# Kernel tuning notes

Measured on AMD Instinct MI355X. Metric: run time of the kernel, lower is better.

The kernel has to match this reference:

```python
import jax, jax.numpy as jnp
import numpy as np

N, D_IN, F1, F2, D_OUT = 10000, 128, 20, 20, 128

def setup_inputs() -> dict:
    key = jax.random.key(0)
    ks = jax.random.split(key, 8)
    x = jax.random.normal(ks[0], (N, D_IN), dtype=jnp.float32)
    adj = jax.random.uniform(ks[1], (N, N), dtype=jnp.float32)
    # Kipf-style GraphConvolution params: W in [in,out], bias [out]
    def glorot(k, fi, fo):
        s = 1.0 / np.sqrt(fi)
        return jax.random.uniform(k, (fi, fo), dtype=jnp.float32, minval=-s, maxval=s)
    W1 = glorot(ks[2], D_IN, F1); b1 = jnp.zeros((F1,), jnp.float32)
    W2 = glorot(ks[3], F1, F2);  b2 = jnp.zeros((F2,), jnp.float32)
    W3 = glorot(ks[4], F2, D_OUT); b3 = jnp.zeros((D_OUT,), jnp.float32)
    return {"x": x, "adj": adj, "W1": W1, "b1": b1, "W2": W2, "b2": b2, "W3": W3, "b3": b3}

def _gcn(h, adj, W, b):
    # GraphConvolution: adj @ (h @ W) + b
    return adj @ (h @ W) + b

def reference(x, adj, W1, b1, W2, b2, W3, b3):
    # eval mode: F.dropout(training=False) is identity
    h = jax.nn.relu(_gcn(x, adj, W1, b1))
    h = jax.nn.relu(_gcn(h, adj, W2, b2))
    h = jax.nn.relu(_gcn(h, adj, W3, b3))
    return jax.nn.relu(h + x)
```

## Files before the change

kernel.cpp:

```cpp
#include <hip/hip_runtime.h>

constexpr int NN   = 10000;
constexpr int DIN  = 128;
constexpr int F    = 20;
constexpr int DOUT = 128;

constexpr int KSPLIT = 25;
constexpr int KRANGE = NN / KSPLIT;
constexpr int TM     = 128;
constexpr int ROWBLK = (NN + TM - 1) / TM;
constexpr int NFLT4  = NN * F / 4;

__global__ __launch_bounds__(256) void gemm_x_w1(const float* __restrict__ x,
                                                 const float* __restrict__ W,
                                                 float* __restrict__ out) {
    int t = blockIdx.x * 256 + threadIdx.x;
    if (t >= NN * F) return;
    int i = t / F, f = t % F;
    const float4* xp = (const float4*)(x + (size_t)i * DIN);
    float s = 0.f;
#pragma unroll
    for (int k4 = 0; k4 < DIN / 4; ++k4) {
        float4 xv = xp[k4];
        int k = k4 * 4;
        s += xv.x * W[(k + 0) * F + f];
        s += xv.y * W[(k + 1) * F + f];
        s += xv.z * W[(k + 2) * F + f];
        s += xv.w * W[(k + 3) * F + f];
    }
    out[t] = s;
}

__global__ __launch_bounds__(256) void gemm_h_w2(const float* __restrict__ h,
                                                 const float* __restrict__ W,
                                                 float* __restrict__ out) {
    int t = blockIdx.x * 256 + threadIdx.x;
    if (t >= NN * F) return;
    int i = t / F, g = t % F;
    const float* hp = h + (size_t)i * F;
    float s = 0.f;
#pragma unroll
    for (int f = 0; f < F; ++f) s += hp[f] * W[f * F + g];
    out[t] = s;
}

__global__ __launch_bounds__(256) void bias_relu(const float* __restrict__ in,
                                                 const float* __restrict__ b,
                                                 float* __restrict__ out) {
    int t = blockIdx.x * 256 + threadIdx.x;
    if (t >= NN * F) return;
    out[t] = fmaxf(in[t] + b[t % F], 0.f);
}

template <int REV, int PART>
__global__ __launch_bounds__(256) void adjmm(const float* __restrict__ adj,
                                             const float* __restrict__ t,
                                             float* __restrict__ out) {
    __shared__ __align__(16) float tl[KRANGE * F];

    const int tid = threadIdx.x;
    const int bx = REV ? ((int)gridDim.x - 1 - (int)blockIdx.x) : (int)blockIdx.x;
    const int by = REV ? ((int)gridDim.y - 1 - (int)blockIdx.y) : (int)blockIdx.y;
    const int row0 = bx * TM;
    const int k0   = by * KRANGE;

    {
        const float4* src = (const float4*)(t + (size_t)k0 * F);
        float4* dst = (float4*)tl;
#pragma unroll
        for (int i = 0; i < 8; ++i) {
            int idx = tid + i * 256;
            if (idx < KRANGE * F / 4) dst[idx] = src[idx];
        }
    }
    __syncthreads();

    const int r   = tid >> 1;
    const int p   = tid & 1;
    const int row = row0 + r;
    if (row < NN) {
        float4 acc[5];
#pragma unroll
        for (int c = 0; c < 5; ++c) acc[c] = make_float4(0.f, 0.f, 0.f, 0.f);

        const float4* ap = (const float4*)(adj + (size_t)row * NN + k0);
#pragma unroll 2
        for (int m = 0; m < KRANGE / 8; ++m) {
            const int mm = REV ? (KRANGE / 8 - 1 - m) : m;
            float4 a = ap[2 * mm + p];
            const float* trow = tl + (8 * mm + 4 * p) * F;
#pragma unroll
            for (int j = 0; j < 4; ++j) {
                const float aj = (j == 0) ? a.x : (j == 1) ? a.y : (j == 2) ? a.z : a.w;
                const float4* tp = (const float4*)(trow + j * F);
#pragma unroll
                for (int c = 0; c < 5; ++c) {
                    float4 tv = tp[c];
                    acc[c].x += aj * tv.x;
                    acc[c].y += aj * tv.y;
                    acc[c].z += aj * tv.z;
                    acc[c].w += aj * tv.w;
                }
            }
        }

#pragma unroll
        for (int c = 0; c < 5; ++c) {
            acc[c].x += __shfl_xor(acc[c].x, 1);
            acc[c].y += __shfl_xor(acc[c].y, 1);
            acc[c].z += __shfl_xor(acc[c].z, 1);
            acc[c].w += __shfl_xor(acc[c].w, 1);
        }

        if (PART) {
            if (p == 0) {
                float4* op = (float4*)(out + ((size_t)by * NN + row) * F);
#pragma unroll
                for (int c = 0; c < 5; ++c) op[c] = acc[c];
            }
        } else {
            if (p == 0) {
                float* op = out + (size_t)row * F;
#pragma unroll
                for (int c = 0; c < 5; ++c) {
                    atomicAdd(op + c * 4 + 0, acc[c].x);
                    atomicAdd(op + c * 4 + 1, acc[c].y);
                    atomicAdd(op + c * 4 + 2, acc[c].z);
                    atomicAdd(op + c * 4 + 3, acc[c].w);
                }
            }
        }
    }
}

template <int BIASRELU>
__global__ __launch_bounds__(256) void reduce_p(const float* __restrict__ P,
                                                const float* __restrict__ b,
                                                float* __restrict__ out) {
    int t = blockIdx.x * 256 + threadIdx.x;
    if (t >= NFLT4) return;
    float4 s = ((const float4*)P)[t];
    for (int k = 1; k < KSPLIT; ++k) {
        float4 v = ((const float4*)P)[(size_t)k * NFLT4 + t];
        s.x += v.x; s.y += v.y; s.z += v.z; s.w += v.w;
    }
    if (BIASRELU) {
        int f4 = t % (F / 4);
        float4 bv = ((const float4*)b)[f4];
        s.x = fmaxf(s.x + bv.x, 0.f);
        s.y = fmaxf(s.y + bv.y, 0.f);
        s.z = fmaxf(s.z + bv.z, 0.f);
        s.w = fmaxf(s.w + bv.w, 0.f);
    }
    ((float4*)out)[t] = s;
}

__global__ __launch_bounds__(256) void final_fuse(const float* __restrict__ u,
                                                  const float* __restrict__ W3,
                                                  const float* __restrict__ b3,
                                                  const float* __restrict__ x,
                                                  float* __restrict__ out) {
    int t = blockIdx.x * 256 + threadIdx.x;
    if (t >= NN * DOUT) return;
    int i = t / DOUT, f = t % DOUT;
    const float* up = u + (size_t)i * F;
    float s = b3[f];
#pragma unroll
    for (int g = 0; g < F; ++g) s += up[g] * W3[g * DOUT + f];
    float h = fmaxf(s, 0.f);
    out[t] = fmaxf(h + x[t], 0.f);
}

extern "C" void kernel_launch(void* const* d_in, const int* in_sizes, int n_in,
                              void* d_out, int out_size, void* d_ws, size_t ws_size,
                              hipStream_t stream) {
    const float* x   = (const float*)d_in[0];
    const float* adj = (const float*)d_in[1];
    const float* W1  = (const float*)d_in[2];
    const float* b1  = (const float*)d_in[3];
    const float* W2  = (const float*)d_in[4];
    const float* b2  = (const float*)d_in[5];
    const float* W3  = (const float*)d_in[6];
    const float* b3  = (const float*)d_in[7];
    float* out = (float*)d_out;

    float* A = (float*)d_ws;
    float* C = A + (size_t)NN * F;
    float* P = C + (size_t)NN * F;
    const size_t nf_bytes = (size_t)NN * F * sizeof(float);
    const size_t need = nf_bytes * (2 + KSPLIT);

    const int blk_nf  = (NN * F + 255) / 256;
    const int blk_nf4 = (NFLT4 + 255) / 256;
    const int blk_no  = (NN * DOUT + 255) / 256;
    dim3 agrid(ROWBLK, KSPLIT);

    if (ws_size >= need) {
        gemm_x_w1<<<blk_nf, 256, 0, stream>>>(x, W1, A);
        adjmm<0, 1><<<agrid, 256, 0, stream>>>(adj, A, P);
        reduce_p<1><<<blk_nf4, 256, 0, stream>>>(P, b1, C);

        gemm_h_w2<<<blk_nf, 256, 0, stream>>>(C, W2, A);
        adjmm<1, 1><<<agrid, 256, 0, stream>>>(adj, A, P);
        reduce_p<1><<<blk_nf4, 256, 0, stream>>>(P, b2, C);

        adjmm<0, 1><<<agrid, 256, 0, stream>>>(adj, C, P);
        reduce_p<0><<<blk_nf4, 256, 0, stream>>>(P, nullptr, A);
        final_fuse<<<blk_no, 256, 0, stream>>>(A, W3, b3, x, out);
    } else {
        float* B = P;
        gemm_x_w1<<<blk_nf, 256, 0, stream>>>(x, W1, A);
        hipMemsetAsync(B, 0, nf_bytes, stream);
        adjmm<0, 0><<<agrid, 256, 0, stream>>>(adj, A, B);
        bias_relu<<<blk_nf, 256, 0, stream>>>(B, b1, C);

        gemm_h_w2<<<blk_nf, 256, 0, stream>>>(C, W2, A);
        hipMemsetAsync(B, 0, nf_bytes, stream);
        adjmm<1, 0><<<agrid, 256, 0, stream>>>(adj, A, B);
        bias_relu<<<blk_nf, 256, 0, stream>>>(B, b2, C);

        hipMemsetAsync(A, 0, nf_bytes, stream);
        adjmm<0, 0><<<agrid, 256, 0, stream>>>(adj, C, A);
        final_fuse<<<blk_no, 256, 0, stream>>>(A, W3, b3, x, out);
    }
}
```

Before: 812.0 us.

## Register-block four rows per thread in adj matmul and halve K range

Each thread now accumulates four adjacency rows, so every LDS read of the t tile feeds four rows of FMAs instead of one. To fit the LDS budget the K split goes from 25 to 50 chunks, which halves the shared tile and doubles the partial-sum buffer that reduce_p must read. Register pressure rises to 80 float accumulators per thread, which may lower occupancy and hurt latency hiding for the bandwidth-bound adj stream. The row tile grows to 512, so there are fewer row blocks per K chunk.

```diff
diff --git a/kernel.cpp b/kernel.cpp
--- a/kernel.cpp
+++ b/kernel.cpp
@@ -5,9 +5,10 @@
 constexpr int F    = 20;
 constexpr int DOUT = 128;
 
-constexpr int KSPLIT = 25;
+constexpr int KSPLIT = 50;
 constexpr int KRANGE = NN / KSPLIT;
-constexpr int TM     = 128;
+constexpr int TM     = 512;
+constexpr int RPT    = 4;
 constexpr int ROWBLK = (NN + TM - 1) / TM;
 constexpr int NFLT4  = NN * F / 4;
 
@@ -68,65 +69,92 @@
         const float4* src = (const float4*)(t + (size_t)k0 * F);
         float4* dst = (float4*)tl;
 #pragma unroll
-        for (int i = 0; i < 8; ++i) {
+        for (int i = 0; i < 4; ++i) {
             int idx = tid + i * 256;
             if (idx < KRANGE * F / 4) dst[idx] = src[idx];
         }
     }
     __syncthreads();
 
-    const int r   = tid >> 1;
-    const int p   = tid & 1;
-    const int row = row0 + r;
-    if (row < NN) {
-        float4 acc[5];
-#pragma unroll
-        for (int c = 0; c < 5; ++c) acc[c] = make_float4(0.f, 0.f, 0.f, 0.f);
-
-        const float4* ap = (const float4*)(adj + (size_t)row * NN + k0);
+    const int r = tid >> 1;
+    const int p = tid & 1;
+
+    int   rows[RPT];
+    bool  ok[RPT];
+    const float4* ap[RPT];
+#pragma unroll
+    for (int c = 0; c < RPT; ++c) {
+        int row = row0 + r + c * 128;
+        ok[c]   = row < NN;
+        rows[c] = ok[c] ? row : (NN - 1);
+        ap[c]   = (const float4*)(adj + (size_t)rows[c] * NN + k0);
+    }
+
+    float4 acc[RPT][5];
+#pragma unroll
+    for (int c = 0; c < RPT; ++c)
+#pragma unroll
+        for (int q = 0; q < 5; ++q) acc[c][q] = make_float4(0.f, 0.f, 0.f, 0.f);
+
+    constexpr int M = KRANGE / 8;
 #pragma unroll 2
-        for (int m = 0; m < KRANGE / 8; ++m) {
-            const int mm = REV ? (KRANGE / 8 - 1 - m) : m;
-            float4 a = ap[2 * mm + p];
-            const float* trow = tl + (8 * mm + 4 * p) * F;
-#pragma unroll
-            for (int j = 0; j < 4; ++j) {
-                const float aj = (j == 0) ? a.x : (j == 1) ? a.y : (j == 2) ? a.z : a.w;
-                const float4* tp = (const float4*)(trow + j * F);
-#pragma unroll
-                for (int c = 0; c < 5; ++c) {
-                    float4 tv = tp[c];
-                    acc[c].x += aj * tv.x;
-                    acc[c].y += aj * tv.y;
-                    acc[c].z += aj * tv.z;
-                    acc[c].w += aj * tv.w;
-                }
+    for (int m = 0; m < M; ++m) {
+        const int mm = REV ? (M - 1 - m) : m;
+        float4 a[RPT];
+#pragma unroll
+        for (int c = 0; c < RPT; ++c) a[c] = ap[c][2 * mm + p];
+#pragma unroll
+        for (int j = 0; j < 4; ++j) {
+            const float4* tp = (const float4*)(tl + (8 * mm + 4 * p + j) * F);
+            float4 tv0 = tp[0], tv1 = tp[1], tv2 = tp[2], tv3 = tp[3], tv4 = tp[4];
+#pragma unroll
+            for (int c = 0; c < RPT; ++c) {
+                const float aj = (j == 0) ? a[c].x : (j == 1) ? a[c].y
+                               : (j == 2) ? a[c].z : a[c].w;
+                acc[c][0].x += aj * tv0.x; acc[c][0].y += aj * tv0.y;
+                acc[c][0].z += aj * tv0.z; acc[c][0].w += aj * tv0.w;
+                acc[c][1].x += aj * tv1.x; acc[c][1].y += aj * tv1.y;
+                acc[c][1].z += aj * tv1.z; acc[c][1].w += aj * tv1.w;
+                acc[c][2].x += aj * tv2.x; acc[c][2].y += aj * tv2.y;
+                acc[c][2].z += aj * tv2.z; acc[c][2].w += aj * tv2.w;
+                acc[c][3].x += aj * tv3.x; acc[c][3].y += aj * tv3.y;
+                acc[c][3].z += aj * tv3.z; acc[c][3].w += aj * tv3.w;
+                acc[c][4].x += aj * tv4.x; acc[c][4].y += aj * tv4.y;
+                acc[c][4].z += aj * tv4.z; acc[c][4].w += aj * tv4.w;
             }
         }
-
-#pragma unroll
-        for (int c = 0; c < 5; ++c) {
-            acc[c].x += __shfl_xor(acc[c].x, 1);
-            acc[c].y += __shfl_xor(acc[c].y, 1);
-            acc[c].z += __shfl_xor(acc[c].z, 1);
-            acc[c].w += __shfl_xor(acc[c].w, 1);
-        }
-
+    }
+
+#pragma unroll
+    for (int c = 0; c < RPT; ++c)
+#pragma unroll
+        for (int q = 0; q < 5; ++q) {
+            acc[c][q].x += __shfl_xor(acc[c][q].x, 1);
+            acc[c][q].y += __shfl_xor(acc[c][q].y, 1);
+            acc[c][q].z += __shfl_xor(acc[c][q].z, 1);
+            acc[c][q].w += __shfl_xor(acc[c][q].w, 1);
+        }
+
+    if (p == 0) {
         if (PART) {
-            if (p == 0) {
-                float4* op = (float4*)(out + ((size_t)by * NN + row) * F);
-#pragma unroll
-                for (int c = 0; c < 5; ++c) op[c] = acc[c];
+#pragma unroll
+            for (int c = 0; c < RPT; ++c) {
+                if (!ok[c]) continue;
+                float4* op = (float4*)(out + ((size_t)by * NN + rows[c]) * F);
+#pragma unroll
+                for (int q = 0; q < 5; ++q) op[q] = acc[c][q];
             }
         } else {
-            if (p == 0) {
-                float* op = out + (size_t)row * F;
-#pragma unroll
-                for (int c = 0; c < 5; ++c) {
-                    atomicAdd(op + c * 4 + 0, acc[c].x);
-                    atomicAdd(op + c * 4 + 1, acc[c].y);
-                    atomicAdd(op + c * 4 + 2, acc[c].z);
-                    atomicAdd(op + c * 4 + 3, acc[c].w);
+#pragma unroll
+            for (int c = 0; c < RPT; ++c) {
+                if (!ok[c]) continue;
+                float* op = out + (size_t)rows[c] * F;
+#pragma unroll
+                for (int q = 0; q < 5; ++q) {
+                    atomicAdd(op + q * 4 + 0, acc[c][q].x);
+                    atomicAdd(op + q * 4 + 1, acc[c][q].y);
+                    atomicAdd(op + q * 4 + 2, acc[c][q].z);
+                    atomicAdd(op + q * 4 + 3, acc[c][q].w);
                 }
             }
         }
```

Result: slower. 919.5 us (+13.2%).

## Double K-split and software-pipeline adj loads in register chunks

Applied to the files above, without the earlier changes.

Doubles the K split to 50, which halves the shared-memory tile per block and allows more resident blocks (launch_bounds occupancy hint of 4). The inner loop is fully unrolled into chunks of 5 float4 adjacency loads, and the next chunk is prefetched into registers while the current one is consumed, so more memory requests are in flight. Out-of-range rows are clamped so all threads take part in the shuffle. The cost is twice as many partial sums to write and reduce, plus higher register pressure from the prefetch buffers.

```diff
diff --git a/kernel.cpp b/kernel.cpp
--- a/kernel.cpp
+++ b/kernel.cpp
@@ -5,11 +5,14 @@
 constexpr int F    = 20;
 constexpr int DOUT = 128;
 
-constexpr int KSPLIT = 25;
+constexpr int KSPLIT = 50;
 constexpr int KRANGE = NN / KSPLIT;
 constexpr int TM     = 128;
 constexpr int ROWBLK = (NN + TM - 1) / TM;
 constexpr int NFLT4  = NN * F / 4;
+constexpr int M      = KRANGE / 8;
+constexpr int CH     = 5;
+constexpr int NCHUNK = M / CH;
 
 __global__ __launch_bounds__(256) void gemm_x_w1(const float* __restrict__ x,
                                                  const float* __restrict__ W,
@@ -53,9 +56,9 @@
 }
 
 template <int REV, int PART>
-__global__ __launch_bounds__(256) void adjmm(const float* __restrict__ adj,
-                                             const float* __restrict__ t,
-                                             float* __restrict__ out) {
+__global__ __launch_bounds__(256, 4) void adjmm(const float* __restrict__ adj,
+                                                const float* __restrict__ t,
+                                                float* __restrict__ out) {
     __shared__ __align__(16) float tl[KRANGE * F];
 
     const int tid = threadIdx.x;
@@ -68,66 +71,87 @@
         const float4* src = (const float4*)(t + (size_t)k0 * F);
         float4* dst = (float4*)tl;
 #pragma unroll
-        for (int i = 0; i < 8; ++i) {
+        for (int i = 0; i < 4; ++i) {
             int idx = tid + i * 256;
             if (idx < KRANGE * F / 4) dst[idx] = src[idx];
         }
     }
     __syncthreads();
 
-    const int r   = tid >> 1;
-    const int p   = tid & 1;
-    const int row = row0 + r;
-    if (row < NN) {
-        float4 acc[5];
-#pragma unroll
-        for (int c = 0; c < 5; ++c) acc[c] = make_float4(0.f, 0.f, 0.f, 0.f);
-
-        const float4* ap = (const float4*)(adj + (size_t)row * NN + k0);
-#pragma unroll 2
-        for (int m = 0; m < KRANGE / 8; ++m) {
-            const int mm = REV ? (KRANGE / 8 - 1 - m) : m;
-            float4 a = ap[2 * mm + p];
-            const float* trow = tl + (8 * mm + 4 * p) * F;
+    const int r = tid >> 1;
+    const int p = tid & 1;
+    const int row  = row0 + r;
+    const bool ok  = row < NN;
+    const int rowc = ok ? row : (NN - 1);
+
+    const float4* ap = (const float4*)(adj + (size_t)rowc * NN + k0);
+
+    float4 acc[5];
+#pragma unroll
+    for (int q = 0; q < 5; ++q) acc[q] = make_float4(0.f, 0.f, 0.f, 0.f);
+
+    auto MIDX = [&](int c, int i) -> int {
+        int m = c * CH + i;
+        return REV ? (M - 1 - m) : m;
+    };
+
+    float4 aC[CH], aN[CH];
+#pragma unroll
+    for (int i = 0; i < CH; ++i) aC[i] = ap[2 * MIDX(0, i) + p];
+
+#pragma unroll
+    for (int c = 0; c < NCHUNK; ++c) {
+        if (c + 1 < NCHUNK) {
+#pragma unroll
+            for (int i = 0; i < CH; ++i) aN[i] = ap[2 * MIDX(c + 1, i) + p];
+        }
+#pragma unroll
+        for (int i = 0; i < CH; ++i) {
+            const int mm = MIDX(c, i);
+            const float4 a = aC[i];
 #pragma unroll
             for (int j = 0; j < 4; ++j) {
-                const float aj = (j == 0) ? a.x : (j == 1) ? a.y : (j == 2) ? a.z : a.w;
-                const float4* tp = (const float4*)(trow + j * F);
-#pragma unroll
-                for (int c = 0; c < 5; ++c) {
-                    float4 tv = tp[c];
-                    acc[c].x += aj * tv.x;
-                    acc[c].y += aj * tv.y;
-                    acc[c].z += aj * tv.z;
-                    acc[c].w += aj * tv.w;
-                }
+                const float aj = (j == 0) ? a.x : (j == 1) ? a.y
+                               : (j == 2) ? a.z : a.w;
+                const float4* tp = (const float4*)(tl + (8 * mm + 4 * p + j) * F);
+                float4 tv0 = tp[0], tv1 = tp[1], tv2 = tp[2], tv3 = tp[3], tv4 = tp[4];
+                acc[0].x += aj * tv0.x; acc[0].y += aj * tv0.y;
+                acc[0].z += aj * tv0.z; acc[0].w += aj * tv0.w;
+                acc[1].x += aj * tv1.x; acc[1].y += aj * tv1.y;
+                acc[1].z += aj * tv1.z; acc[1].w += aj * tv1.w;
+                acc[2].x += aj * tv2.x; acc[2].y += aj * tv2.y;
+                acc[2].z += aj * tv2.z; acc[2].w += aj * tv2.w;
+                acc[3].x += aj * tv3.x; acc[3].y += aj * tv3.y;
+                acc[3].z += aj * tv3.z; acc[3].w += aj * tv3.w;
+                acc[4].x += aj * tv4.x; acc[4].y += aj * tv4.y;
+                acc[4].z += aj * tv4.z; acc[4].w += aj * tv4.w;
             }
         }
-
-#pragma unroll
-        for (int c = 0; c < 5; ++c) {
-            acc[c].x += __shfl_xor(acc[c].x, 1);
-            acc[c].y += __shfl_xor(acc[c].y, 1);
-            acc[c].z += __shfl_xor(acc[c].z, 1);
-            acc[c].w += __shfl_xor(acc[c].w, 1);
-        }
-
+#pragma unroll
+        for (int i = 0; i < CH; ++i) aC[i] = aN[i];
+    }
+
+#pragma unroll
+    for (int q = 0; q < 5; ++q) {
+        acc[q].x += __shfl_xor(acc[q].x, 1);
+        acc[q].y += __shfl_xor(acc[q].y, 1);
+        acc[q].z += __shfl_xor(acc[q].z, 1);
+        acc[q].w += __shfl_xor(acc[q].w, 1);
+    }
+
+    if (p == 0 && ok) {
         if (PART) {
-            if (p == 0) {
-                float4* op = (float4*)(out + ((size_t)by * NN + row) * F);
-#pragma unroll
-                for (int c = 0; c < 5; ++c) op[c] = acc[c];
-            }
+            float4* op = (float4*)(out + ((size_t)by * NN + row) * F);
+#pragma unroll
+            for (int q = 0; q < 5; ++q) op[q] = acc[q];
         } else {
-            if (p == 0) {
-                float* op = out + (size_t)row * F;
-#pragma unroll
-                for (int c = 0; c < 5; ++c) {
-                    atomicAdd(op + c * 4 + 0, acc[c].x);
-                    atomicAdd(op + c * 4 + 1, acc[c].y);
-                    atomicAdd(op + c * 4 + 2, acc[c].z);
-                    atomicAdd(op + c * 4 + 3, acc[c].w);
-                }
+            float* op = out + (size_t)row * F;
+#pragma unroll
+            for (int q = 0; q < 5; ++q) {
+                atomicAdd(op + q * 4 + 0, acc[q].x);
+                atomicAdd(op + q * 4 + 1, acc[q].y);
+                atomicAdd(op + q * 4 + 2, acc[q].z);
+                atomicAdd(op + q * 4 + 3, acc[q].w);
             }
         }
     }
```

After: 839.0 us. 1.03x slower.
